# Kernel optimization log

Hardware: AMD Instinct MI355X
Metric: run time of the kernel (lower is better)

Reference implementation:

```python
import jax, jax.numpy as jnp
import numpy as np

MAX_CONTEXT = 100
NUM_HEADS = 4
GRU_GROUPS = 4


def _layernorm(x, g, b, eps=1e-5):
    m = jnp.mean(x, axis=-1, keepdims=True)
    v = jnp.mean((x - m) ** 2, axis=-1, keepdims=True)
    return (x - m) / jnp.sqrt(v + eps) * g + b


def _grouped_gru(x, wih, whh, bih, bhh, G):
    # x: [N, T, C]; shared GRU params run on each channel group (PyTorch gate order r,z,n)
    N, T, C = x.shape
    D = C // G
    xg = x.reshape(N, T, G, D)
    xp = jnp.einsum('ntgd,ed->ntge', xg, wih) + bih  # e = 3D, precomputed input projections
    xp = jnp.moveaxis(xp, 1, 0)  # [T, N, G, 3D]

    def step(h, xt):
        gh = jnp.einsum('ngd,ed->nge', h, whh) + bhh
        xr, xz, xn = jnp.split(xt, 3, axis=-1)
        hr, hz, hn = jnp.split(gh, 3, axis=-1)
        r = jax.nn.sigmoid(xr + hr)
        z = jax.nn.sigmoid(xz + hz)
        n = jnp.tanh(xn + r * hn)
        h = (1.0 - z) * n + z * h
        return h, h

    h0 = jnp.zeros((N, G, D), x.dtype)
    _, hs = jax.lax.scan(step, h0, xp)  # hs: [T, N, G, D]
    return jnp.moveaxis(hs, 0, 1).reshape(N, T, C)


def _mha(x, wqkv, bqkv, wo, bo, H, max_ctx):
    # batch_first self-attention with causal + truncated-window additive mask
    N, T, C = x.shape
    Dh = C // H
    qkv = x @ wqkv.T + bqkv
    q, k, v = jnp.split(qkv, 3, axis=-1)
    q = q.reshape(N, T, H, Dh)
    k = k.reshape(N, T, H, Dh)
    v = v.reshape(N, T, H, Dh)
    scale = 1.0 / np.sqrt(Dh).astype(np.float32)
    scores = jnp.einsum('nqhd,nkhd->nhqk', q, k) * scale
    i = jnp.arange(T)
    diff = i[:, None] - i[None, :]
    allowed = (diff >= 0) & (diff <= max_ctx)
    scores = jnp.where(allowed, scores, -jnp.inf)
    attn = jax.nn.softmax(scores, axis=-1)
    out = jnp.einsum('nhqk,nkhd->nqhd', attn, v).reshape(N, T, C)
    return out @ wo.T + bo


def setup_inputs() -> dict:
    key = jax.random.key(0)
    ks = jax.random.split(key, 5)
    B, C, T, F = 2, 128, 512, 64
    D = C // GRU_GROUPS
    s = 0.1
    return {
        'x': jax.random.normal(ks[0], (B, C, T, F), jnp.float32),
        'ln1_g': jnp.ones((C,), jnp.float32),
        'ln1_b': jnp.zeros((C,), jnp.float32),
        'gru_wih': jax.random.normal(ks[1], (3 * D, D), jnp.float32) * s,
        'gru_whh': jax.random.normal(ks[2], (3 * D, D), jnp.float32) * s,
        'gru_bih': jnp.zeros((3 * D,), jnp.float32),
        'gru_bhh': jnp.zeros((3 * D,), jnp.float32),
        'ln2_g': jnp.ones((C,), jnp.float32),
        'ln2_b': jnp.zeros((C,), jnp.float32),
        'in_proj_w': jax.random.normal(ks[3], (3 * C, C), jnp.float32) * s,
        'in_proj_b': jnp.zeros((3 * C,), jnp.float32),
        'out_proj_w': jax.random.normal(ks[4], (C, C), jnp.float32) * s,
        'out_proj_b': jnp.zeros((C,), jnp.float32),
    }


def reference(x, ln1_g, ln1_b, gru_wih, gru_whh, gru_bih, gru_bhh, ln2_g, ln2_b, in_proj_w, in_proj_b, out_proj_w, out_proj_b):
    B, C, T, F = x.shape
    # [B, C, T, F] -> [B*F, T, C]: each freq bin is an independent time sequence
    seq = jnp.transpose(x, (0, 3, 2, 1)).reshape(B * F, T, C)
    seq = seq + _grouped_gru(_layernorm(seq, ln1_g, ln1_b), gru_wih, gru_whh, gru_bih, gru_bhh, GRU_GROUPS)
    seq = seq + _mha(_layernorm(seq, ln2_g, ln2_b), in_proj_w, in_proj_b, out_proj_w, out_proj_b, NUM_HEADS, MAX_CONTEXT)
    return jnp.transpose(seq.reshape(B, F, T, C), (0, 3, 2, 1))
```

## Files before the change

### kernel.cpp

```cpp
#include <hip/hip_runtime.h>
#include <hip/hip_bf16.h>
#include <math.h>


typedef __attribute__((ext_vector_type(8))) short short8;
typedef __attribute__((ext_vector_type(4))) float f32x4;
typedef __attribute__((ext_vector_type(2))) float f32x2;

__device__ __forceinline__ float bflo(unsigned int u) { return __uint_as_float(u << 16); }
__device__ __forceinline__ float bfhi(unsigned int u) { return __uint_as_float(u & 0xffff0000u); }
__device__ __forceinline__ float bf2f(unsigned short u) { return __uint_as_float(((unsigned int)u) << 16); }
__device__ __forceinline__ unsigned short f2bf(float f) {
  __hip_bfloat16 h = __float2bfloat16(f);
  return *reinterpret_cast<unsigned short*>(&h);
}

typedef __attribute__((address_space(1))) const unsigned int uint_g;
typedef __attribute__((address_space(3))) unsigned int uint_l;
__device__ __forceinline__ void glds16(const void* g, void* l) {
  __builtin_amdgcn_global_load_lds((uint_g*)g, (uint_l*)l, 16, 0, 0);
}

__global__ void cvt_kernel(const float* __restrict__ s, unsigned short* __restrict__ d, int n) {
  int i = blockIdx.x * 256 + threadIdx.x;
  if (i < n) d[i] = f2bf(s[i]);
}

__global__ __launch_bounds__(256) void transpose_in_kernel(const float* __restrict__ x, float* __restrict__ seq) {
  __shared__ float tile[128 * 65];
  int b = blockIdx.x >> 9;
  int t = blockIdx.x & 511;
  for (int i = threadIdx.x; i < 128 * 64; i += 256) {
    int c = i >> 6, f = i & 63;
    tile[c * 65 + f] = x[(((size_t)(b * 128 + c)) * 512 + t) * 64 + f];
  }
  __syncthreads();
  for (int i = threadIdx.x; i < 64 * 128; i += 256) {
    int f = i >> 7, c = i & 127;
    seq[(((size_t)(b * 64 + f)) * 512 + t) * 128 + c] = tile[c * 65 + f];
  }
}

__global__ __launch_bounds__(256) void transpose_out_kernel(const float* __restrict__ seq, float* __restrict__ out) {
  __shared__ float tile[128 * 65];
  int b = blockIdx.x >> 9;
  int t = blockIdx.x & 511;
  for (int i = threadIdx.x; i < 64 * 128; i += 256) {
    int f = i >> 7, c = i & 127;
    tile[c * 65 + f] = seq[(((size_t)(b * 64 + f)) * 512 + t) * 128 + c];
  }
  __syncthreads();
  for (int i = threadIdx.x; i < 128 * 64; i += 256) {
    int c = i >> 6, f = i & 63;
    out[(((size_t)(b * 128 + c)) * 512 + t) * 64 + f] = tile[c * 65 + f];
  }
}

__global__ __launch_bounds__(256) void ln_kernel(const float* __restrict__ in, const float* __restrict__ g,
                                                 const float* __restrict__ b, unsigned short* __restrict__ out) {
  int row = blockIdx.x * 4 + (threadIdx.x >> 6);
  int lane = threadIdx.x & 63;
  float2 v = ((const float2*)(in + (size_t)row * 128))[lane];
  float s = v.x + v.y, ss = v.x * v.x + v.y * v.y;
  #pragma unroll
  for (int off = 32; off > 0; off >>= 1) {
    s += __shfl_xor(s, off);
    ss += __shfl_xor(ss, off);
  }
  float mean = s * (1.f / 128.f);
  float var = ss * (1.f / 128.f) - mean * mean;
  float rs = rsqrtf(var + 1e-5f);
  float2 gg = ((const float2*)g)[lane];
  float2 bb = ((const float2*)b)[lane];
  float o0 = (v.x - mean) * rs * gg.x + bb.x;
  float o1 = (v.y - mean) * rs * gg.y + bb.y;
  unsigned int packed = ((unsigned int)f2bf(o1) << 16) | (unsigned int)f2bf(o0);
  ((unsigned int*)(out + (size_t)row * 128))[lane] = packed;
}

template <int K, int MODE>
__global__ __launch_bounds__(256) void gemm_mfma(const unsigned short* __restrict__ A,
                                                 const unsigned short* __restrict__ W,
                                                 const float* __restrict__ bias,
                                                 unsigned short* __restrict__ outB,
                                                 float* __restrict__ outF, int Ncols) {
  const int tid = threadIdx.x;
  const int wave = tid >> 6, lane = tid & 63;
  const int wy = wave >> 1, wx = wave & 1;
  const int lr = lane & 15, lq = lane >> 4;
  const int m0 = blockIdx.x * 128 + wy * 64;
  const int n0 = blockIdx.y * 128 + wx * 64;

  f32x4 acc[4][4];
  #pragma unroll
  for (int i = 0; i < 4; ++i)
    #pragma unroll
    for (int j = 0; j < 4; ++j) acc[i][j] = f32x4{0.f, 0.f, 0.f, 0.f};

  const short8 zfrag = short8{0, 0, 0, 0, 0, 0, 0, 0};

  #pragma unroll
  for (int kk = 0; kk < K; kk += 32) {
    short8 af[4], bfq[4];
    #pragma unroll
    for (int i = 0; i < 4; ++i)
      af[i] = *(const short8*)(A + (size_t)(m0 + i * 16 + lr) * K + kk + lq * 8);
    #pragma unroll
    for (int j = 0; j < 4; ++j) {
      int wr = n0 + j * 16 + lr;
      bfq[j] = (wr < Ncols) ? *(const short8*)(W + (size_t)wr * K + kk + lq * 8) : zfrag;
    }
    #pragma unroll
    for (int i = 0; i < 4; ++i)
      #pragma unroll
      for (int j = 0; j < 4; ++j)
        acc[i][j] = __builtin_amdgcn_mfma_f32_16x16x32_bf16(af[i], bfq[j], acc[i][j], 0, 0, 0);
  }

  #pragma unroll
  for (int j = 0; j < 4; ++j) {
    int col = n0 + j * 16 + lr;
    if (col < Ncols) {
      float bb = bias[col];
      #pragma unroll
      for (int i = 0; i < 4; ++i) {
        #pragma unroll
        for (int r = 0; r < 4; ++r) {
          int row = m0 + i * 16 + lq * 4 + r;
          float v = acc[i][j][r] + bb;
          if (MODE == 0)
            outB[(size_t)row * Ncols + col] = f2bf(v);
          else
            outF[(size_t)row * 128 + col] += v;
        }
      }
    }
  }
}

__global__ __launch_bounds__(64, 1) void gru_kernel(const unsigned short* __restrict__ xp,
                                                    const float* __restrict__ whh,
                                                    const float* __restrict__ bhh,
                                                    float* __restrict__ seq) {
  const int l = threadIdx.x;
  const int half = l >> 5, d = l & 31;
  const int blk = blockIdx.x;
  const int chain = blk * 2 + half;
  const int n = chain >> 2;
  const int g0 = (blk * 2) & 3;

  const float LOG2E = 1.4426950408889634f;
  const float T2LOG2E = 2.8853900817779268f;

  __shared__ __align__(16) unsigned char stage[2][6144];
  __shared__ __align__(16) float h_lds[2][64];
  h_lds[0][l] = 0.f;

  f32x2 wr2[16], wz2[16], wn2[16];
  #pragma unroll
  for (int u = 0; u < 16; ++u) {
    float2 a = *(const float2*)(whh + (size_t)d * 32 + u * 2);
    float2 b = *(const float2*)(whh + (size_t)(32 + d) * 32 + u * 2);
    float2 c = *(const float2*)(whh + (size_t)(64 + d) * 32 + u * 2);
    wr2[u] = f32x2{a.x * LOG2E, a.y * LOG2E};
    wz2[u] = f32x2{b.x * LOG2E, b.y * LOG2E};
    wn2[u] = f32x2{c.x * T2LOG2E, c.y * T2LOG2E};
  }
  #pragma unroll
  for (int u = 0; u < 16; ++u)
    asm volatile("" : "+v"(wr2[u]), "+v"(wz2[u]), "+v"(wn2[u]));

  float br = bhh[d] * LOG2E, bz = bhh[32 + d] * LOG2E, bn = bhh[64 + d] * T2LOG2E;
  asm volatile("" : "+v"(br), "+v"(bz), "+v"(bn));

  const char* xg = (const char*)xp;
  const size_t cb0 = ((size_t)n * 2048 + g0) * 192;
  const size_t cb1 = ((size_t)n * 2048 + g0 + 1) * 192;
  const int fa = l * 16;
  const int oxa = (fa / 192) * 768 + (fa % 192);
  const int fb = 1024 + l * 16;
  const int oxb = (fb / 192) * 768 + (fb % 192);
  const char* px0a = xg + cb0 + oxa;
  const char* px0b = xg + cb0 + oxb;
  const char* px1a = xg + cb1 + oxa;
  const char* px1b = xg + cb1 + oxb;
  const int osa = (l >> 4) * 512 + (l & 15) * 16;
  const size_t sqb0 = ((size_t)n * 512 * 128 + (size_t)g0 * 32) * 4;
  const char* psa = (const char*)seq + sqb0 + osa;
  const char* psb = psa + 2048;

  float* sb = seq + (size_t)n * 512 * 128 + g0 * 32 + l;

  glds16(px0a, stage[0] + 0);
  glds16(px0b, stage[0] + 1024);
  glds16(px1a, stage[0] + 2048);
  glds16(px1b, stage[0] + 3072);
  glds16(psa,  stage[0] + 4096);
  glds16(psb,  stage[0] + 5120);

  float hprev = 0.f;

  for (int c = 0; c < 64; ++c) {
    const int cur = c & 1;
    if (c < 63) {
      const size_t xo = (size_t)(c + 1) * 6144;
      const size_t so = (size_t)(c + 1) * 4096;
      unsigned char* nb = stage[cur ^ 1];
      glds16(px0a + xo, nb + 0);
      glds16(px0b + xo, nb + 1024);
      glds16(px1a + xo, nb + 2048);
      glds16(px1b + xo, nb + 3072);
      glds16(psa + so,  nb + 4096);
      glds16(psb + so,  nb + 5120);
    }
    __builtin_amdgcn_sched_barrier(0);
    if (c == 0)       asm volatile("s_waitcnt vmcnt(6)" ::: "memory");
    else if (c == 63) asm volatile("s_waitcnt vmcnt(8)" ::: "memory");
    else              asm volatile("s_waitcnt vmcnt(14)" ::: "memory");
    __builtin_amdgcn_sched_barrier(0);

    const unsigned char* scur = stage[cur];
    #pragma unroll
    for (int p = 0; p < 8; ++p) {
      const int t = c * 8 + p;

      const f32x4* hsrc = (const f32x4*)&h_lds[p & 1][half * 32];
      f32x2 ar0 = f32x2{br, 0.f}, ar1 = f32x2{0.f, 0.f};
      f32x2 az0 = f32x2{bz, 0.f}, az1 = f32x2{0.f, 0.f};
      f32x2 an0 = f32x2{bn, 0.f}, an1 = f32x2{0.f, 0.f};
      #pragma unroll
      for (int u = 0; u < 8; ++u) {
        f32x4 h4 = hsrc[u];
        f32x2 hlo = f32x2{h4.x, h4.y};
        f32x2 hhi = f32x2{h4.z, h4.w};
        ar0 += wr2[2 * u] * hlo; ar1 += wr2[2 * u + 1] * hhi;
        az0 += wz2[2 * u] * hlo; az1 += wz2[2 * u + 1] * hhi;
        an0 += wn2[2 * u] * hlo; an1 += wn2[2 * u + 1] * hhi;
      }
      f32x2 arv = ar0 + ar1, azv = az0 + az1, anv = an0 + an1;
      float accr = arv.x + arv.y;
      float accz = azv.x + azv.y;
      float accn = anv.x + anv.y;

      const unsigned short* xrow = (const unsigned short*)(scur + half * 2048 + p * 192);
      float xr = bf2f(xrow[d]) * LOG2E;
      float xz = bf2f(xrow[32 + d]) * LOG2E;
      float xn2 = bf2f(xrow[64 + d]) * T2LOG2E;
      float sv0 = *(const float*)(scur + 4096 + p * 256 + (l << 2));

      float r = __builtin_amdgcn_rcpf(1.f + __builtin_amdgcn_exp2f(-(xr + accr)));
      float z = __builtin_amdgcn_rcpf(1.f + __builtin_amdgcn_exp2f(-(xz + accz)));
      float e2 = __builtin_amdgcn_exp2f(xn2 + r * accn);
      float nn = 1.f - 2.f * __builtin_amdgcn_rcpf(e2 + 1.f);
      float hnew = z * (hprev - nn) + nn;
      hprev = hnew;

      h_lds[(p + 1) & 1][l] = hnew;
      sb[(size_t)t * 128] = sv0 + hnew;
    }
  }
}

__global__ __launch_bounds__(256) void attn_kernel(const unsigned short* __restrict__ qkv,
                                                   unsigned short* __restrict__ outp) {
  const int qbase = blockIdx.x * 64;
  const int h = blockIdx.y;
  const int n = blockIdx.z;
  const int tid = threadIdx.x;
  const int w = tid >> 6, lane = tid & 63;
  const int lr = lane & 15, lq = lane >> 4;
  const int ws0 = max(0, qbase - 100);

  const int KROWS = 192;
  const int VPITCH = 200;
  const int PPITCH = 40;

  __shared__ unsigned short KL[192 * 32];
  __shared__ unsigned short VT[32 * 200];
  __shared__ unsigned short PL[4][16 * 40];
  __shared__ float LL[64];

  const char* qkvb = (const char*)qkv;
  const size_t rowb = ((size_t)(n * 512 + ws0)) * 768;

  const int wq0 = qbase + w * 16;
  short8 qfrag = *(const short8*)(qkvb + ((size_t)(n * 512 + wq0 + lr)) * 768 + h * 64 + lq * 16);

  #pragma unroll
  for (int it = 0; it < 3; ++it) {
    int c = w * 192 + it * 64 + lane;
    const char* src = qkvb + rowb + (size_t)(c >> 2) * 768 + 256 + h * 64 + (size_t)(c & 3) * 16;
    glds16(src, (char*)KL + w * 3072 + it * 1024);
  }

  if (tid < KROWS) {
    const unsigned int* vsrc = (const unsigned int*)(qkvb + rowb + (size_t)tid * 768 + 512 + h * 64);
    #pragma unroll
    for (int u = 0; u < 16; ++u) {
      unsigned int vv = vsrc[u];
      VT[(2 * u) * VPITCH + tid] = (unsigned short)(vv & 0xffff);
      VT[(2 * u + 1) * VPITCH + tid] = (unsigned short)(vv >> 16);
    }
  }
  __syncthreads();

  const float SCL2 = 0.17677669529663687f * 1.4426950408889634f;
  const int lo = max(0, wq0 - 100) - ws0;
  const int hi = wq0 + 15 - ws0;
  const int kc0 = lo >> 5, kc1 = hi >> 5;

  f32x4 oacc0 = f32x4{0.f, 0.f, 0.f, 0.f};
  f32x4 oacc1 = f32x4{0.f, 0.f, 0.f, 0.f};
  float lsum[4] = {0.f, 0.f, 0.f, 0.f};
  unsigned short* plw = PL[w];

  for (int kc = kc0; kc <= kc1; ++kc) {
    #pragma unroll
    for (int sub = 0; sub < 2; ++sub) {
      const int kt = kc * 2 + sub;
      short8 kfrag = *(const short8*)(KL + (kt * 16 + lr) * 32 + lq * 8);
      f32x4 s4 = __builtin_amdgcn_mfma_f32_16x16x32_bf16(qfrag, kfrag,
                                                         f32x4{0.f, 0.f, 0.f, 0.f}, 0, 0, 0);
      const int tk = ws0 + kt * 16 + lr;
      #pragma unroll
      for (int r = 0; r < 4; ++r) {
        const int tq = wq0 + lq * 4 + r;
        bool ok = (tk <= tq) && (tk + 100 >= tq);
        float p = ok ? __builtin_amdgcn_exp2f(s4[r] * SCL2) : 0.f;
        lsum[r] += p;
        plw[(lq * 4 + r) * PPITCH + sub * 16 + lr] = f2bf(p);
      }
    }
    short8 pfrag = *(const short8*)(plw + lr * PPITCH + lq * 8);
    short8 vf0 = *(const short8*)(VT + lr * VPITCH + kc * 32 + lq * 8);
    short8 vf1 = *(const short8*)(VT + (16 + lr) * VPITCH + kc * 32 + lq * 8);
    oacc0 = __builtin_amdgcn_mfma_f32_16x16x32_bf16(vf0, pfrag, oacc0, 0, 0, 0);
    oacc1 = __builtin_amdgcn_mfma_f32_16x16x32_bf16(vf1, pfrag, oacc1, 0, 0, 0);
  }

  #pragma unroll
  for (int r = 0; r < 4; ++r) {
    float v = lsum[r];
    v += __shfl_xor(v, 1); v += __shfl_xor(v, 2);
    v += __shfl_xor(v, 4); v += __shfl_xor(v, 8);
    lsum[r] = v;
  }
  if (lr == 0) {
    #pragma unroll
    for (int r = 0; r < 4; ++r) LL[w * 16 + lq * 4 + r] = lsum[r];
  }
  float rl = __builtin_amdgcn_rcpf(LL[w * 16 + lr]);

  unsigned short* ob = outp + ((size_t)(n * 512 + wq0 + lr)) * 128 + h * 32 + lq * 4;
  {
    unsigned int w0 = ((unsigned int)f2bf(oacc0[1] * rl) << 16) | f2bf(oacc0[0] * rl);
    unsigned int w1 = ((unsigned int)f2bf(oacc0[3] * rl) << 16) | f2bf(oacc0[2] * rl);
    uint2 pk0; pk0.x = w0; pk0.y = w1;
    *(uint2*)ob = pk0;
    unsigned int w2 = ((unsigned int)f2bf(oacc1[1] * rl) << 16) | f2bf(oacc1[0] * rl);
    unsigned int w3 = ((unsigned int)f2bf(oacc1[3] * rl) << 16) | f2bf(oacc1[2] * rl);
    uint2 pk1; pk1.x = w2; pk1.y = w3;
    *(uint2*)(ob + 16) = pk1;
  }
}

extern "C" void kernel_launch(void* const* d_in, const int* in_sizes, int n_in,
                              void* d_out, int out_size, void* d_ws, size_t ws_size,
                              hipStream_t stream) {
  const float* x      = (const float*)d_in[0];
  const float* ln1_g  = (const float*)d_in[1];
  const float* ln1_b  = (const float*)d_in[2];
  const float* wih    = (const float*)d_in[3];
  const float* whh    = (const float*)d_in[4];
  const float* bih    = (const float*)d_in[5];
  const float* bhh    = (const float*)d_in[6];
  const float* ln2_g  = (const float*)d_in[7];
  const float* ln2_b  = (const float*)d_in[8];
  const float* inw    = (const float*)d_in[9];
  const float* inb    = (const float*)d_in[10];
  const float* outw   = (const float*)d_in[11];
  const float* outb   = (const float*)d_in[12];

  char* ws = (char*)d_ws;
  float*          seq   = (float*)ws;
  unsigned short* tmpb  = (unsigned short*)(ws + 33554432);
  unsigned short* big   = (unsigned short*)(ws + 50331648);
  unsigned short* wih_b = (unsigned short*)(ws + 100663296);
  unsigned short* inw_b = wih_b + 3072;
  unsigned short* outw_b = inw_b + 49152;

  cvt_kernel<<<12, 256, 0, stream>>>(wih, wih_b, 3072);
  cvt_kernel<<<192, 256, 0, stream>>>(inw, inw_b, 49152);
  cvt_kernel<<<64, 256, 0, stream>>>(outw, outw_b, 16384);

  transpose_in_kernel<<<1024, 256, 0, stream>>>(x, seq);

  ln_kernel<<<16384, 256, 0, stream>>>(seq, ln1_g, ln1_b, tmpb);

  gemm_mfma<32, 0><<<dim3(2048, 1), 256, 0, stream>>>(tmpb, wih_b, bih, big, nullptr, 96);

  gru_kernel<<<256, 64, 0, stream>>>(big, whh, bhh, seq);

  ln_kernel<<<16384, 256, 0, stream>>>(seq, ln2_g, ln2_b, tmpb);

  gemm_mfma<128, 0><<<dim3(512, 3), 256, 0, stream>>>(tmpb, inw_b, inb, big, nullptr, 384);

  attn_kernel<<<dim3(8, 4, 128), 256, 0, stream>>>(big, tmpb);

  gemm_mfma<128, 1><<<dim3(512, 1), 256, 0, stream>>>(tmpb, outw_b, outb, nullptr, seq, 128);

  transpose_out_kernel<<<1024, 256, 0, stream>>>(seq, (float*)d_out);
}
```

Before: 370.7 us.

## Broadcast GRU hidden state via DPP/swizzle instead of LDS round-trip

The GRU recurrence no longer writes each step's hidden state to shared memory and reads it back as vectors. Each lane now holds two h values, its own and its 16-lane partner's obtained via ds_swizzle. The matvec rotates them through DPP permutations, with the weight registers pre-permuted to match the XOR access pattern. The x-projection and residual loads for all 8 steps in a chunk are also hoisted out of the serial loop. The goal is to cut the LDS latency on the critical dependency chain of the sequential scan, at the cost of more DPP moves and a more intricate lane mapping.

```diff
diff --git a/kernel.cpp b/kernel.cpp
--- a/kernel.cpp
+++ b/kernel.cpp
@@ -19,6 +19,13 @@
 typedef __attribute__((address_space(3))) unsigned int uint_l;
 __device__ __forceinline__ void glds16(const void* g, void* l) {
   __builtin_amdgcn_global_load_lds((uint_g*)g, (uint_l*)l, 16, 0, 0);
+}
+
+template <int CTRL>
+__device__ __forceinline__ f32x2 dpp2(f32x2 v) {
+  int a = __builtin_amdgcn_mov_dpp(__float_as_int(v.x), CTRL, 0xF, 0xF, false);
+  int b = __builtin_amdgcn_mov_dpp(__float_as_int(v.y), CTRL, 0xF, 0xF, false);
+  return f32x2{__int_as_float(a), __int_as_float(b)};
 }
 
 __global__ void cvt_kernel(const float* __restrict__ s, unsigned short* __restrict__ d, int n) {
@@ -144,6 +151,7 @@
                                                     float* __restrict__ seq) {
   const int l = threadIdx.x;
   const int half = l >> 5, d = l & 31;
+  const int cc = l & 15, rm = (l >> 4) & 1;
   const int blk = blockIdx.x;
   const int chain = blk * 2 + half;
   const int n = chain >> 2;
@@ -153,22 +161,19 @@
   const float T2LOG2E = 2.8853900817779268f;
 
   __shared__ __align__(16) unsigned char stage[2][6144];
-  __shared__ __align__(16) float h_lds[2][64];
-  h_lds[0][l] = 0.f;
 
   f32x2 wr2[16], wz2[16], wn2[16];
   #pragma unroll
-  for (int u = 0; u < 16; ++u) {
-    float2 a = *(const float2*)(whh + (size_t)d * 32 + u * 2);
-    float2 b = *(const float2*)(whh + (size_t)(32 + d) * 32 + u * 2);
-    float2 c = *(const float2*)(whh + (size_t)(64 + d) * 32 + u * 2);
-    wr2[u] = f32x2{a.x * LOG2E, a.y * LOG2E};
-    wz2[u] = f32x2{b.x * LOG2E, b.y * LOG2E};
-    wn2[u] = f32x2{c.x * T2LOG2E, c.y * T2LOG2E};
-  }
-  #pragma unroll
-  for (int u = 0; u < 16; ++u)
-    asm volatile("" : "+v"(wr2[u]), "+v"(wz2[u]), "+v"(wn2[u]));
+  for (int k = 0; k < 16; ++k) {
+    int jA = rm * 16 + (cc ^ k);
+    int jB = (1 - rm) * 16 + (cc ^ k);
+    wr2[k] = f32x2{whh[(size_t)d * 32 + jA] * LOG2E, whh[(size_t)d * 32 + jB] * LOG2E};
+    wz2[k] = f32x2{whh[(size_t)(32 + d) * 32 + jA] * LOG2E, whh[(size_t)(32 + d) * 32 + jB] * LOG2E};
+    wn2[k] = f32x2{whh[(size_t)(64 + d) * 32 + jA] * T2LOG2E, whh[(size_t)(64 + d) * 32 + jB] * T2LOG2E};
+  }
+  #pragma unroll
+  for (int k = 0; k < 16; ++k)
+    asm volatile("" : "+v"(wr2[k]), "+v"(wz2[k]), "+v"(wn2[k]));
 
   float br = bhh[d] * LOG2E, bz = bhh[32 + d] * LOG2E, bn = bhh[64 + d] * T2LOG2E;
   asm volatile("" : "+v"(br), "+v"(bz), "+v"(bn));
@@ -199,6 +204,7 @@
   glds16(psb,  stage[0] + 5120);
 
   float hprev = 0.f;
+  f32x2 h2cur = f32x2{0.f, 0.f};
 
   for (int c = 0; c < 64; ++c) {
     const int cur = c & 1;
@@ -220,43 +226,55 @@
     __builtin_amdgcn_sched_barrier(0);
 
     const unsigned char* scur = stage[cur];
+    float pxr[8], pxz[8], pxn[8], psv[8];
+    #pragma unroll
+    for (int p = 0; p < 8; ++p) {
+      const unsigned short* xrow = (const unsigned short*)(scur + half * 2048 + p * 192);
+      pxr[p] = bf2f(xrow[d]) * LOG2E;
+      pxz[p] = bf2f(xrow[32 + d]) * LOG2E;
+      pxn[p] = bf2f(xrow[64 + d]) * T2LOG2E;
+      psv[p] = *(const float*)(scur + 4096 + p * 256 + (l << 2));
+    }
+
     #pragma unroll
     for (int p = 0; p < 8; ++p) {
       const int t = c * 8 + p;
 
-      const f32x4* hsrc = (const f32x4*)&h_lds[p & 1][half * 32];
-      f32x2 ar0 = f32x2{br, 0.f}, ar1 = f32x2{0.f, 0.f};
-      f32x2 az0 = f32x2{bz, 0.f}, az1 = f32x2{0.f, 0.f};
-      f32x2 an0 = f32x2{bn, 0.f}, an1 = f32x2{0.f, 0.f};
-      #pragma unroll
-      for (int u = 0; u < 8; ++u) {
-        f32x4 h4 = hsrc[u];
-        f32x2 hlo = f32x2{h4.x, h4.y};
-        f32x2 hhi = f32x2{h4.z, h4.w};
-        ar0 += wr2[2 * u] * hlo; ar1 += wr2[2 * u + 1] * hhi;
-        az0 += wz2[2 * u] * hlo; az1 += wz2[2 * u + 1] * hhi;
-        an0 += wn2[2 * u] * hlo; an1 += wn2[2 * u + 1] * hhi;
-      }
-      f32x2 arv = ar0 + ar1, azv = az0 + az1, anv = an0 + an1;
-      float accr = arv.x + arv.y;
-      float accz = azv.x + azv.y;
-      float accn = anv.x + anv.y;
-
-      const unsigned short* xrow = (const unsigned short*)(scur + half * 2048 + p * 192);
-      float xr = bf2f(xrow[d]) * LOG2E;
-      float xz = bf2f(xrow[32 + d]) * LOG2E;
-      float xn2 = bf2f(xrow[64 + d]) * T2LOG2E;
-      float sv0 = *(const float*)(scur + 4096 + p * 256 + (l << 2));
-
-      float r = __builtin_amdgcn_rcpf(1.f + __builtin_amdgcn_exp2f(-(xr + accr)));
-      float z = __builtin_amdgcn_rcpf(1.f + __builtin_amdgcn_exp2f(-(xz + accz)));
-      float e2 = __builtin_amdgcn_exp2f(xn2 + r * accn);
+      f32x2 h2 = h2cur;
+      f32x2 ar = f32x2{br, 0.f}, az = f32x2{bz, 0.f}, an = f32x2{bn, 0.f};
+#define MV(K) ar += wr2[K] * h2; az += wz2[K] * h2; an += wn2[K] * h2;
+      MV(0)  h2 = dpp2<0xB1>(h2);
+      MV(1)  h2 = dpp2<0x1B>(h2);
+      MV(2)  h2 = dpp2<0xB1>(h2);
+      MV(3)  h2 = dpp2<0x141>(h2);
+      MV(4)  h2 = dpp2<0xB1>(h2);
+      MV(5)  h2 = dpp2<0x1B>(h2);
+      MV(6)  h2 = dpp2<0xB1>(h2);
+      MV(7)  h2 = dpp2<0x140>(h2);
+      MV(8)  h2 = dpp2<0xB1>(h2);
+      MV(9)  h2 = dpp2<0x1B>(h2);
+      MV(10) h2 = dpp2<0xB1>(h2);
+      MV(11) h2 = dpp2<0x141>(h2);
+      MV(12) h2 = dpp2<0xB1>(h2);
+      MV(13) h2 = dpp2<0x1B>(h2);
+      MV(14) h2 = dpp2<0xB1>(h2);
+      MV(15)
+#undef MV
+      float accr = ar.x + ar.y;
+      float accz = az.x + az.y;
+      float accn = an.x + an.y;
+
+      float r = __builtin_amdgcn_rcpf(1.f + __builtin_amdgcn_exp2f(-(pxr[p] + accr)));
+      float z = __builtin_amdgcn_rcpf(1.f + __builtin_amdgcn_exp2f(-(pxz[p] + accz)));
+      float e2 = __builtin_amdgcn_exp2f(pxn[p] + r * accn);
       float nn = 1.f - 2.f * __builtin_amdgcn_rcpf(e2 + 1.f);
       float hnew = z * (hprev - nn) + nn;
       hprev = hnew;
 
-      h_lds[(p + 1) & 1][l] = hnew;
-      sb[(size_t)t * 128] = sv0 + hnew;
+      int hb = __builtin_amdgcn_ds_swizzle(__float_as_int(hnew), 0x401F);
+      h2cur = f32x2{hnew, __int_as_float(hb)};
+
+      sb[(size_t)t * 128] = psv[p] + hnew;
     }
   }
 }
```

New measurement: 376.7 us. Within noise of the previous version (+1.6%).

## Split GRU recurrent dot product across wave halves, one chain per wave

Applied to the files above, without the earlier changes.

The GRU kernel now gives each 64-lane wave a single recurrence chain instead of two. Each half-wave computes half of the 32-element recurrent dot product, and the halves are combined with a cross-half shuffle. This shortens the serial per-step matvec and halves the weight registers per lane, aiming to cut the latency of each of the 512 sequential steps. The cost is extra shuffle latency on every step and a grid twice as large, with half the lanes doing redundant gate math. Staging buffers and vmcnt waits are resized to match.

```diff
diff --git a/kernel.cpp b/kernel.cpp
--- a/kernel.cpp
+++ b/kernel.cpp
@@ -143,60 +143,55 @@
                                                     const float* __restrict__ bhh,
                                                     float* __restrict__ seq) {
   const int l = threadIdx.x;
-  const int half = l >> 5, d = l & 31;
-  const int blk = blockIdx.x;
-  const int chain = blk * 2 + half;
-  const int n = chain >> 2;
-  const int g0 = (blk * 2) & 3;
+  const int jh = l >> 5;
+  const int d = l & 31;
+  const int chain = blockIdx.x;
+  const int n = chain >> 2, g = chain & 3;
 
   const float LOG2E = 1.4426950408889634f;
   const float T2LOG2E = 2.8853900817779268f;
 
-  __shared__ __align__(16) unsigned char stage[2][6144];
-  __shared__ __align__(16) float h_lds[2][64];
-  h_lds[0][l] = 0.f;
-
-  f32x2 wr2[16], wz2[16], wn2[16];
-  #pragma unroll
-  for (int u = 0; u < 16; ++u) {
-    float2 a = *(const float2*)(whh + (size_t)d * 32 + u * 2);
-    float2 b = *(const float2*)(whh + (size_t)(32 + d) * 32 + u * 2);
-    float2 c = *(const float2*)(whh + (size_t)(64 + d) * 32 + u * 2);
+  __shared__ __align__(16) unsigned char stage[2][3072];
+  __shared__ __align__(16) float h_lds[2][32];
+  if (l < 32) { h_lds[0][l] = 0.f; h_lds[1][l] = 0.f; }
+  __builtin_amdgcn_wave_barrier();
+
+  f32x2 wr2[8], wz2[8], wn2[8];
+  #pragma unroll
+  for (int u = 0; u < 8; ++u) {
+    const float* base = whh + (size_t)d * 32 + jh * 16 + u * 2;
+    float2 a = *(const float2*)(base);
+    float2 b = *(const float2*)(base + 1024);
+    float2 c = *(const float2*)(base + 2048);
     wr2[u] = f32x2{a.x * LOG2E, a.y * LOG2E};
     wz2[u] = f32x2{b.x * LOG2E, b.y * LOG2E};
     wn2[u] = f32x2{c.x * T2LOG2E, c.y * T2LOG2E};
   }
   #pragma unroll
-  for (int u = 0; u < 16; ++u)
+  for (int u = 0; u < 8; ++u)
     asm volatile("" : "+v"(wr2[u]), "+v"(wz2[u]), "+v"(wn2[u]));
 
-  float br = bhh[d] * LOG2E, bz = bhh[32 + d] * LOG2E, bn = bhh[64 + d] * T2LOG2E;
+  float br = jh ? 0.f : bhh[d] * LOG2E;
+  float bz = jh ? 0.f : bhh[32 + d] * LOG2E;
+  float bn = jh ? 0.f : bhh[64 + d] * T2LOG2E;
   asm volatile("" : "+v"(br), "+v"(bz), "+v"(bn));
 
   const char* xg = (const char*)xp;
-  const size_t cb0 = ((size_t)n * 2048 + g0) * 192;
-  const size_t cb1 = ((size_t)n * 2048 + g0 + 1) * 192;
-  const int fa = l * 16;
-  const int oxa = (fa / 192) * 768 + (fa % 192);
-  const int fb = 1024 + l * 16;
-  const int oxb = (fb / 192) * 768 + (fb % 192);
-  const char* px0a = xg + cb0 + oxa;
-  const char* px0b = xg + cb0 + oxb;
-  const char* px1a = xg + cb1 + oxa;
-  const char* px1b = xg + cb1 + oxb;
-  const int osa = (l >> 4) * 512 + (l & 15) * 16;
-  const size_t sqb0 = ((size_t)n * 512 * 128 + (size_t)g0 * 32) * 4;
-  const char* psa = (const char*)seq + sqb0 + osa;
-  const char* psb = psa + 2048;
-
-  float* sb = seq + (size_t)n * 512 * 128 + g0 * 32 + l;
-
-  glds16(px0a, stage[0] + 0);
-  glds16(px0b, stage[0] + 1024);
-  glds16(px1a, stage[0] + 2048);
-  glds16(px1b, stage[0] + 3072);
-  glds16(psa,  stage[0] + 4096);
-  glds16(psb,  stage[0] + 5120);
+  const size_t cbase = ((size_t)n * 2048 + g) * 192;
+  const int f0 = l * 16;
+  const int ox0 = (f0 / 192) * 768 + (f0 % 192);
+  const int f1 = 1024 + l * 16;
+  const int ox1 = (f1 / 192) * 768 + (f1 % 192);
+  const char* pxa = xg + cbase + ox0;
+  const char* pxb = xg + cbase + ox1;
+  const int osa = (l >> 3) * 512 + (l & 7) * 16;
+  const char* psa = (const char*)seq + ((size_t)n * 512 * 128 + (size_t)g * 32) * 4 + osa;
+
+  float* sb = seq + (size_t)n * 512 * 128 + g * 32 + d;
+
+  glds16(pxa, stage[0] + 0);
+  glds16(pxb, stage[0] + 1024);
+  glds16(psa, stage[0] + 2048);
 
   float hprev = 0.f;
 
@@ -206,17 +201,14 @@
       const size_t xo = (size_t)(c + 1) * 6144;
       const size_t so = (size_t)(c + 1) * 4096;
       unsigned char* nb = stage[cur ^ 1];
-      glds16(px0a + xo, nb + 0);
-      glds16(px0b + xo, nb + 1024);
-      glds16(px1a + xo, nb + 2048);
-      glds16(px1b + xo, nb + 3072);
-      glds16(psa + so,  nb + 4096);
-      glds16(psb + so,  nb + 5120);
+      glds16(pxa + xo, nb + 0);
+      glds16(pxb + xo, nb + 1024);
+      glds16(psa + so, nb + 2048);
     }
     __builtin_amdgcn_sched_barrier(0);
-    if (c == 0)       asm volatile("s_waitcnt vmcnt(6)" ::: "memory");
+    if (c == 0)       asm volatile("s_waitcnt vmcnt(3)" ::: "memory");
     else if (c == 63) asm volatile("s_waitcnt vmcnt(8)" ::: "memory");
-    else              asm volatile("s_waitcnt vmcnt(14)" ::: "memory");
+    else              asm volatile("s_waitcnt vmcnt(11)" ::: "memory");
     __builtin_amdgcn_sched_barrier(0);
 
     const unsigned char* scur = stage[cur];
@@ -224,29 +216,32 @@
     for (int p = 0; p < 8; ++p) {
       const int t = c * 8 + p;
 
-      const f32x4* hsrc = (const f32x4*)&h_lds[p & 1][half * 32];
-      f32x2 ar0 = f32x2{br, 0.f}, ar1 = f32x2{0.f, 0.f};
-      f32x2 az0 = f32x2{bz, 0.f}, az1 = f32x2{0.f, 0.f};
-      f32x2 an0 = f32x2{bn, 0.f}, an1 = f32x2{0.f, 0.f};
+      const f32x4* hsrc = (const f32x4*)&h_lds[p & 1][jh * 16];
+      f32x2 a0 = f32x2{br, 0.f}, a1 = f32x2{0.f, 0.f};
+      f32x2 z0 = f32x2{bz, 0.f}, z1 = f32x2{0.f, 0.f};
+      f32x2 q0 = f32x2{bn, 0.f}, q1 = f32x2{0.f, 0.f};
       #pragma unroll
-      for (int u = 0; u < 8; ++u) {
+      for (int u = 0; u < 4; ++u) {
         f32x4 h4 = hsrc[u];
         f32x2 hlo = f32x2{h4.x, h4.y};
         f32x2 hhi = f32x2{h4.z, h4.w};
-        ar0 += wr2[2 * u] * hlo; ar1 += wr2[2 * u + 1] * hhi;
-        az0 += wz2[2 * u] * hlo; az1 += wz2[2 * u + 1] * hhi;
-        an0 += wn2[2 * u] * hlo; an1 += wn2[2 * u + 1] * hhi;
+        a0 += wr2[2 * u] * hlo; a1 += wr2[2 * u + 1] * hhi;
+        z0 += wz2[2 * u] * hlo; z1 += wz2[2 * u + 1] * hhi;
+        q0 += wn2[2 * u] * hlo; q1 += wn2[2 * u + 1] * hhi;
       }
-      f32x2 arv = ar0 + ar1, azv = az0 + az1, anv = an0 + an1;
-      float accr = arv.x + arv.y;
-      float accz = azv.x + azv.y;
-      float accn = anv.x + anv.y;
-
-      const unsigned short* xrow = (const unsigned short*)(scur + half * 2048 + p * 192);
+      f32x2 av = a0 + a1, zv = z0 + z1, qv = q0 + q1;
+      float accr = av.x + av.y;
+      float accz = zv.x + zv.y;
+      float accn = qv.x + qv.y;
+      accr += __shfl_xor(accr, 32);
+      accz += __shfl_xor(accz, 32);
+      accn += __shfl_xor(accn, 32);
+
+      const unsigned short* xrow = (const unsigned short*)(scur + p * 192);
       float xr = bf2f(xrow[d]) * LOG2E;
       float xz = bf2f(xrow[32 + d]) * LOG2E;
       float xn2 = bf2f(xrow[64 + d]) * T2LOG2E;
-      float sv0 = *(const float*)(scur + 4096 + p * 256 + (l << 2));
+      float sv0 = *(const float*)(scur + 2048 + p * 128 + (d << 2));
 
       float r = __builtin_amdgcn_rcpf(1.f + __builtin_amdgcn_exp2f(-(xr + accr)));
       float z = __builtin_amdgcn_rcpf(1.f + __builtin_amdgcn_exp2f(-(xz + accz)));
@@ -255,8 +250,8 @@
       float hnew = z * (hprev - nn) + nn;
       hprev = hnew;
 
-      h_lds[(p + 1) & 1][l] = hnew;
-      sb[(size_t)t * 128] = sv0 + hnew;
+      h_lds[(p + 1) & 1][d] = hnew;
+      if (jh == 0) sb[(size_t)t * 128] = sv0 + hnew;
     }
   }
 }
@@ -399,7 +394,7 @@
 
   gemm_mfma<32, 0><<<dim3(2048, 1), 256, 0, stream>>>(tmpb, wih_b, bih, big, nullptr, 96);
 
-  gru_kernel<<<256, 64, 0, stream>>>(big, whh, bhh, seq);
+  gru_kernel<<<512, 64, 0, stream>>>(big, whh, bhh, seq);
 
   ln_kernel<<<16384, 256, 0, stream>>>(seq, ln2_g, ln2_b, tmpb);
 
```

After: 381.8 us. 3.0% more time.
